# Kernel optimization log

Measured on AMD Instinct MI355X. Metric: run time of the kernel, lower is better.

## Reference

```python
import jax, jax.numpy as jnp
import numpy as np
import math

N_WIRES = 8  # fixed by _QuantumHead; embed_dim == n_wires == 8
NUM_HEADS = 4
HEAD_DIM = N_WIRES // NUM_HEADS


def _apply_cnot(state, ctrl, tgt):
    # state: (N, 2,2,...,2); wire w lives on axis w+1.
    c_ax, t_ax = ctrl + 1, tgt + 1
    s0 = jax.lax.index_in_dim(state, 0, c_ax, keepdims=True)
    s1 = jax.lax.index_in_dim(state, 1, c_ax, keepdims=True)
    s1 = jnp.flip(s1, axis=t_ax)  # flip target where control == 1
    return jnp.concatenate([s0, s1], axis=c_ax)


def quantum_head(x_flat, theta):
    """Batched statevector sim of the _QuantumHead circuit.
    x_flat: (N, 8) rx encoding angles; theta: (8,) trainable RX params.
    RX(x_i) then RX(theta_i) on the same wire compose to RX(x_i + theta_i).
    Returns PauliZ expectations per wire: (N, 8).
    """
    n = x_flat.shape[0]
    state = jnp.zeros((n,) + (2,) * N_WIRES, jnp.complex64)
    state = state.at[(slice(None),) + (0,) * N_WIRES].set(1.0)  # |0...0>
    ang = (x_flat + theta[None, :]) * 0.5
    c, s = jnp.cos(ang), jnp.sin(ang)
    for w in range(N_WIRES):
        ax = w + 1
        a0 = jax.lax.index_in_dim(state, 0, ax, keepdims=False)
        a1 = jax.lax.index_in_dim(state, 1, ax, keepdims=False)
        bshape = (-1,) + (1,) * (N_WIRES - 1)
        cw = c[:, w].reshape(bshape)
        sw = s[:, w].reshape(bshape)
        n0 = cw * a0 - 1j * sw * a1
        n1 = -1j * sw * a0 + cw * a1
        state = jnp.stack([n0, n1], axis=ax)
    for w in range(N_WIRES - 1):
        state = _apply_cnot(state, w, w + 1)
    state = _apply_cnot(state, N_WIRES - 1, 0)
    probs = jnp.real(state * jnp.conj(state))
    outs = []
    for w in range(N_WIRES):
        axes = tuple(a for a in range(1, N_WIRES + 1) if a != w + 1)
        zz = probs.sum(axis=axes)  # (N, 2)
        outs.append(zz[:, 0] - zz[:, 1])
    return jnp.stack(outs, axis=-1)


def setup_inputs() -> dict:
    key = jax.random.key(0)
    k1, k2, k3 = jax.random.split(key, 3)
    B, S, E = 16, 1024, N_WIRES
    x = jax.random.normal(k1, (B, S, E), dtype=jnp.float32)
    mask = jnp.ones((B, S), dtype=jnp.int32)
    theta = jax.random.normal(k2, (E,), dtype=jnp.float32)
    w_out = jax.random.normal(k3, (E, E), dtype=jnp.float32) * (1.0 / math.sqrt(E))
    return {"x": x, "mask": mask, "theta": theta, "w_out": w_out}


def reference(x, mask, theta, w_out):
    B, S, E = x.shape
    # q, k, v are all _apply_quantum(x) with shared parameters -> identical.
    qkv = quantum_head(x.reshape(B * S, E), theta).reshape(B, S, E)
    h = qkv.reshape(B, S, NUM_HEADS, HEAD_DIM).transpose(0, 2, 1, 3)  # (B,H,S,d)
    scores = jnp.einsum("bhqd,bhkd->bhqk", h, h) / math.sqrt(HEAD_DIM)
    scores = jnp.where(mask[:, None, None, :] == 0, -jnp.inf, scores)
    attn = jax.nn.softmax(scores, axis=-1)  # dropout is identity in eval
    out = jnp.einsum("bhqk,bhkd->bhqd", attn, h)
    out = out.transpose(0, 2, 1, 3).reshape(B, S, E)
    return out @ w_out.T
```

## Files before the change

### kernel.cpp

```cpp
#include <hip/hip_runtime.h>

#define BB 16
#define SS 1024
#define NW 8
#define QB 64
#define PS 1032

typedef float v2f __attribute__((ext_vector_type(2)));

__global__ __launch_bounds__(1024)
void mhaq_kernel(const float* __restrict__ x,
                 const int*   __restrict__ mask,
                 const float* __restrict__ theta,
                 const float* __restrict__ wout,
                 float* __restrict__ out)
{
    __shared__ float P[8 * PS];
    __shared__ float Qf[QB][NW];
    __shared__ float O[QB][NW];
    __shared__ float W[NW * NW];

    const int tid = threadIdx.x;
    const int b   = blockIdx.x >> 4;
    const int qc  = blockIdx.x & 15;

    float th[NW];
#pragma unroll
    for (int e = 0; e < NW; ++e) th[e] = theta[e];

    {
        const float* xr = x + ((size_t)b * SS + tid) * NW;
        const float4 r0 = *reinterpret_cast<const float4*>(xr);
        const float4 r1 = *reinterpret_cast<const float4*>(xr + 4);
        float g[NW];
        g[0] = __cosf(r0.x + th[0]); g[1] = __cosf(r0.y + th[1]);
        g[2] = __cosf(r0.z + th[2]); g[3] = __cosf(r0.w + th[3]);
        g[4] = __cosf(r1.x + th[4]); g[5] = __cosf(r1.y + th[5]);
        g[6] = __cosf(r1.z + th[6]); g[7] = __cosf(r1.w + th[7]);
        float h[NW];
        h[1] = g[0] * g[1]; h[2] = h[1] * g[2]; h[3] = h[2] * g[3];
        h[4] = h[3] * g[4]; h[5] = h[4] * g[5]; h[6] = h[5] * g[6];
        h[7] = h[6] * g[7];
        h[0] = (g[1] * g[2]) * (g[3] * g[4]) * ((g[5] * g[6]) * g[7]);
        const float mf = (mask[b * SS + tid] != 0) ? 1.0f : 0.0f;
#pragma unroll
        for (int p = 0; p < 4; ++p) {
            P[p * PS + tid]       = h[2 * p]     * mf;
            P[(4 + p) * PS + tid] = h[2 * p + 1] * mf;
        }
        const int r = tid - qc * QB;
        if ((unsigned)r < (unsigned)QB) {
            const float CF = 0.70710678118654752f * 1.44269504088896340f;
#pragma unroll
            for (int w = 0; w < NW; ++w) Qf[r][w] = h[w] * CF;
        }
        if (tid < NW * NW) W[tid] = wout[tid];
        const int cm = __syncthreads_count(mf == 0.0f);

        const int qg = tid >> 6;
        const int hd = (tid >> 4) & 3;
        const int ks = tid & 15;

        float qu[4], qv[4];
#pragma unroll
        for (int i = 0; i < 4; ++i) {
            qu[i] = Qf[qg * 4 + i][2 * hd];
            qv[i] = Qf[qg * 4 + i][2 * hd + 1];
        }

        v2f vd[4], va0[4], va1[4];
#pragma unroll
        for (int i = 0; i < 4; ++i) { vd[i] = (v2f){0.f, 0.f}; va0[i] = (v2f){0.f, 0.f}; va1[i] = (v2f){0.f, 0.f}; }

        const int base0 = hd * PS + 4 * ks;
#pragma unroll
        for (int t = 0; t < 16; ++t) {
            const int a = base0 + 64 * t;
            const float4 Ur = *reinterpret_cast<const float4*>(&P[a]);
            const float4 Vr = *reinterpret_cast<const float4*>(&P[4 * PS + a]);
            const v2f ulo = (v2f){Ur.x, Ur.y}, uhi = (v2f){Ur.z, Ur.w};
            const v2f vlo = (v2f){Vr.x, Vr.y}, vhi = (v2f){Vr.z, Vr.w};
#pragma unroll
            for (int i = 0; i < 4; ++i) {
                const v2f qup = (v2f){qu[i], qu[i]};
                const v2f qvp = (v2f){qv[i], qv[i]};
                const v2f slo = __builtin_elementwise_fma(qup, ulo, qvp * vlo);
                const v2f shi = __builtin_elementwise_fma(qup, uhi, qvp * vhi);
                const v2f wlo = (v2f){__builtin_amdgcn_exp2f(slo.x), __builtin_amdgcn_exp2f(slo.y)};
                const v2f whi = (v2f){__builtin_amdgcn_exp2f(shi.x), __builtin_amdgcn_exp2f(shi.y)};
                vd[i]  += wlo + whi;
                va0[i] = __builtin_elementwise_fma(wlo, ulo, va0[i]);
                va0[i] = __builtin_elementwise_fma(whi, uhi, va0[i]);
                va1[i] = __builtin_elementwise_fma(wlo, vlo, va1[i]);
                va1[i] = __builtin_elementwise_fma(whi, vhi, va1[i]);
            }
        }

        float dd[4], a0[4], a1[4];
#pragma unroll
        for (int i = 0; i < 4; ++i) {
            dd[i] = vd[i].x + vd[i].y;
            a0[i] = va0[i].x + va0[i].y;
            a1[i] = va1[i].x + va1[i].y;
        }
#pragma unroll
        for (int m = 1; m <= 8; m <<= 1) {
#pragma unroll
            for (int i = 0; i < 4; ++i) {
                dd[i] += __shfl_xor(dd[i], m);
                a0[i] += __shfl_xor(a0[i], m);
                a1[i] += __shfl_xor(a1[i], m);
            }
        }
        if (ks == 0) {
#pragma unroll
            for (int i = 0; i < 4; ++i) {
                const float inv = 1.0f / (dd[i] - (float)cm);
                O[qg * 4 + i][2 * hd]     = a0[i] * inv;
                O[qg * 4 + i][2 * hd + 1] = a1[i] * inv;
            }
        }
    }
    __syncthreads();

    if (tid < QB * NW) {
        const int q = tid >> 3, e = tid & 7;
        float s = 0.f;
#pragma unroll
        for (int f = 0; f < NW; ++f) s = __builtin_fmaf(O[q][f], W[e * NW + f], s);
        out[((size_t)(b * SS + qc * QB + q)) * NW + e] = s;
    }
}

extern "C" void kernel_launch(void* const* d_in, const int* in_sizes, int n_in,
                              void* d_out, int out_size, void* d_ws, size_t ws_size,
                              hipStream_t stream) {
    const float* x     = (const float*)d_in[0];
    const int*   mask  = (const int*)d_in[1];
    const float* theta = (const float*)d_in[2];
    const float* wout  = (const float*)d_in[3];
    float* out = (float*)d_out;

    dim3 grid(BB * (SS / QB));
    dim3 block(1024);
    mhaq_kernel<<<grid, block, 0, stream>>>(x, mask, theta, wout, out);
}
```

Before: 17.76 us.

## Replace per-pair exp softmax with truncated Taylor moment expansion over keys

The exact exp(q·k) softmax is replaced by a degree-8 Taylor expansion of the exponential. This lets each head precompute 55 key-moment sums (powers of u and v, weighted by v components for the numerator) once. Each query then evaluates a small polynomial against those moments, so the per-query-key exp and FMA work is gone. The block shrinks from 1024 to 256 threads with 4 rows per thread. The trade-offs are a truncation error bound that relies on |q·k| staying small (which holds since values are products of cosines), plus extra shuffle reductions and more serial synchronisation stages.

Measured after the change: 15.28 us, median of 2. 14.0% less time.

```diff
diff --git a/kernel.cpp b/kernel.cpp
--- a/kernel.cpp
+++ b/kernel.cpp
@@ -4,32 +4,36 @@
 #define SS 1024
 #define NW 8
 #define QB 64
-#define PS 1032
+#define NH 4
 
-typedef float v2f __attribute__((ext_vector_type(2)));
-
-__global__ __launch_bounds__(1024)
-void mhaq_kernel(const float* __restrict__ x,
-                 const int*   __restrict__ mask,
-                 const float* __restrict__ theta,
-                 const float* __restrict__ wout,
-                 float* __restrict__ out)
+__global__ __launch_bounds__(256)
+void mhaq_one(const float* __restrict__ x, const int* __restrict__ mask,
+              const float* __restrict__ theta, const float* __restrict__ wout,
+              float* __restrict__ out)
 {
-    __shared__ float P[8 * PS];
-    __shared__ float Qf[QB][NW];
-    __shared__ float O[QB][NW];
-    __shared__ float W[NW * NW];
+    __shared__ float2 P[NH][SS];
+    __shared__ float  Qf[QB][NW];
+    __shared__ float  O[QB][NW];
+    __shared__ float  W[64];
+    __shared__ float  Traw[NH][55];
+    __shared__ float  Ts[NH][9][12], Ta[NH][9][12], Tb[NH][9][12];
+    __shared__ int    CMcnt;
 
     const int tid = threadIdx.x;
     const int b   = blockIdx.x >> 4;
     const int qc  = blockIdx.x & 15;
 
+    if (tid == 0) CMcnt = 0;
+
     float th[NW];
 #pragma unroll
     for (int e = 0; e < NW; ++e) th[e] = theta[e];
 
-    {
-        const float* xr = x + ((size_t)b * SS + tid) * NW;
+    int localMasked = 0;
+#pragma unroll
+    for (int c = 0; c < 4; ++c) {
+        const int row = tid + 256 * c;
+        const float* xr = x + ((size_t)b * SS + row) * NW;
         const float4 r0 = *reinterpret_cast<const float4*>(xr);
         const float4 r1 = *reinterpret_cast<const float4*>(xr + 4);
         float g[NW];
@@ -42,93 +46,108 @@
         h[4] = h[3] * g[4]; h[5] = h[4] * g[5]; h[6] = h[5] * g[6];
         h[7] = h[6] * g[7];
         h[0] = (g[1] * g[2]) * (g[3] * g[4]) * ((g[5] * g[6]) * g[7]);
-        const float mf = (mask[b * SS + tid] != 0) ? 1.0f : 0.0f;
+        const float mf = (mask[b * SS + row] != 0) ? 1.0f : 0.0f;
+        localMasked += (mf == 0.0f) ? 1 : 0;
 #pragma unroll
-        for (int p = 0; p < 4; ++p) {
-            P[p * PS + tid]       = h[2 * p]     * mf;
-            P[(4 + p) * PS + tid] = h[2 * p + 1] * mf;
+        for (int hd = 0; hd < NH; ++hd)
+            P[hd][row] = make_float2(h[2 * hd] * mf, h[2 * hd + 1] * mf);
+        const int r = row - qc * QB;
+        if ((unsigned)r < (unsigned)QB) {
+            *reinterpret_cast<float4*>(&Qf[r][0]) = make_float4(h[0], h[1], h[2], h[3]);
+            *reinterpret_cast<float4*>(&Qf[r][4]) = make_float4(h[4], h[5], h[6], h[7]);
         }
-        const int r = tid - qc * QB;
-        if ((unsigned)r < (unsigned)QB) {
-            const float CF = 0.70710678118654752f * 1.44269504088896340f;
+    }
+    if (localMasked) atomicAdd(&CMcnt, localMasked);
+    if (tid < 64) W[tid] = wout[tid];
+    __syncthreads();
+
+    {
+        const int hd = tid >> 6, lane = tid & 63;
+        float acc[55];
 #pragma unroll
-            for (int w = 0; w < NW; ++w) Qf[r][w] = h[w] * CF;
-        }
-        if (tid < NW * NW) W[tid] = wout[tid];
-        const int cm = __syncthreads_count(mf == 0.0f);
-
-        const int qg = tid >> 6;
-        const int hd = (tid >> 4) & 3;
-        const int ks = tid & 15;
-
-        float qu[4], qv[4];
+        for (int m = 1; m < 55; ++m) acc[m] = 0.0f;
+#pragma unroll 4
+        for (int c = 0; c < 16; ++c) {
+            const float2 uv = P[hd][c * 64 + lane];
+            float muj[10], mvi[10];
+            muj[0] = 1.0f; muj[1] = uv.x;
+            mvi[0] = 1.0f; mvi[1] = uv.y;
 #pragma unroll
-        for (int i = 0; i < 4; ++i) {
-            qu[i] = Qf[qg * 4 + i][2 * hd];
-            qv[i] = Qf[qg * 4 + i][2 * hd + 1];
-        }
-
-        v2f vd[4], va0[4], va1[4];
+            for (int j = 2; j <= 9; ++j) { muj[j] = muj[j - 1] * uv.x; mvi[j] = mvi[j - 1] * uv.y; }
 #pragma unroll
-        for (int i = 0; i < 4; ++i) { vd[i] = (v2f){0.f, 0.f}; va0[i] = (v2f){0.f, 0.f}; va1[i] = (v2f){0.f, 0.f}; }
-
-        const int base0 = hd * PS + 4 * ks;
+            for (int s = 1; s <= 9; ++s)
 #pragma unroll
-        for (int t = 0; t < 16; ++t) {
-            const int a = base0 + 64 * t;
-            const float4 Ur = *reinterpret_cast<const float4*>(&P[a]);
-            const float4 Vr = *reinterpret_cast<const float4*>(&P[4 * PS + a]);
-            const v2f ulo = (v2f){Ur.x, Ur.y}, uhi = (v2f){Ur.z, Ur.w};
-            const v2f vlo = (v2f){Vr.x, Vr.y}, vhi = (v2f){Vr.z, Vr.w};
-#pragma unroll
-            for (int i = 0; i < 4; ++i) {
-                const v2f qup = (v2f){qu[i], qu[i]};
-                const v2f qvp = (v2f){qv[i], qv[i]};
-                const v2f slo = __builtin_elementwise_fma(qup, ulo, qvp * vlo);
-                const v2f shi = __builtin_elementwise_fma(qup, uhi, qvp * vhi);
-                const v2f wlo = (v2f){__builtin_amdgcn_exp2f(slo.x), __builtin_amdgcn_exp2f(slo.y)};
-                const v2f whi = (v2f){__builtin_amdgcn_exp2f(shi.x), __builtin_amdgcn_exp2f(shi.y)};
-                vd[i]  += wlo + whi;
-                va0[i] = __builtin_elementwise_fma(wlo, ulo, va0[i]);
-                va0[i] = __builtin_elementwise_fma(whi, uhi, va0[i]);
-                va1[i] = __builtin_elementwise_fma(wlo, vlo, va1[i]);
-                va1[i] = __builtin_elementwise_fma(whi, vhi, va1[i]);
-            }
-        }
-
-        float dd[4], a0[4], a1[4];
-#pragma unroll
-        for (int i = 0; i < 4; ++i) {
-            dd[i] = vd[i].x + vd[i].y;
-            a0[i] = va0[i].x + va0[i].y;
-            a1[i] = va1[i].x + va1[i].y;
+                for (int j = 0; j <= s; ++j)
+                    acc[s * (s + 1) / 2 + j] =
+                        __builtin_fmaf(muj[j], mvi[s - j], acc[s * (s + 1) / 2 + j]);
         }
 #pragma unroll
-        for (int m = 1; m <= 8; m <<= 1) {
+        for (int st = 1; st <= 32; st <<= 1)
 #pragma unroll
-            for (int i = 0; i < 4; ++i) {
-                dd[i] += __shfl_xor(dd[i], m);
-                a0[i] += __shfl_xor(a0[i], m);
-                a1[i] += __shfl_xor(a1[i], m);
-            }
-        }
-        if (ks == 0) {
+            for (int m = 1; m < 55; ++m) acc[m] += __shfl_xor(acc[m], st);
+        if (lane == 0) {
+            Traw[hd][0] = (float)(SS - CMcnt);
 #pragma unroll
-            for (int i = 0; i < 4; ++i) {
-                const float inv = 1.0f / (dd[i] - (float)cm);
-                O[qg * 4 + i][2 * hd]     = a0[i] * inv;
-                O[qg * 4 + i][2 * hd + 1] = a1[i] * inv;
-            }
+            for (int m = 1; m < 55; ++m) Traw[hd][m] = acc[m];
         }
     }
     __syncthreads();
 
-    if (tid < QB * NW) {
-        const int q = tid >> 3, e = tid & 7;
-        float s = 0.f;
+    if (tid < NH * 45) {
+        const int hh = tid / 45;
+        int mm = tid % 45, s = 0;
+        while (mm > s) { mm -= s + 1; ++s; }
+        const int j = mm, i = s - mm;
+        float fj = 1.0f, fi = 1.0f;
+        for (int t = 2; t <= j; ++t) fj *= (float)t;
+        for (int t = 2; t <= i; ++t) fi *= (float)t;
+        const float invf = 1.0f / (fj * fi);
+        const int id0 = s * (s + 1) / 2 + j;
+        const int ida = (s + 1) * (s + 2) / 2 + (j + 1);
+        const int idb = (s + 1) * (s + 2) / 2 + j;
+        Ts[hh][j][i] = Traw[hh][id0] * invf;
+        Ta[hh][j][i] = Traw[hh][ida] * invf;
+        Tb[hh][j][i] = Traw[hh][idb] * invf;
+    }
+    __syncthreads();
+
+    {
+        const int q  = tid >> 2;
+        const int hh = tid & 3;
+        const float CF = 0.70710678118654752f;
+        const float qfu = Qf[q][2 * hh] * CF;
+        const float qfv = Qf[q][2 * hh + 1] * CF;
+        float pu[9], pv[9];
+        pu[0] = 1.0f; pv[0] = 1.0f;
 #pragma unroll
-        for (int f = 0; f < NW; ++f) s = __builtin_fmaf(O[q][f], W[e * NW + f], s);
-        out[((size_t)(b * SS + qc * QB + q)) * NW + e] = s;
+        for (int j = 1; j <= 8; ++j) { pu[j] = pu[j - 1] * qfu; pv[j] = pv[j - 1] * qfv; }
+        float d = 0.0f, a0 = 0.0f, a1 = 0.0f;
+#pragma unroll
+        for (int s = 0; s <= 8; ++s)
+#pragma unroll
+            for (int j = 0; j <= s; ++j) {
+                const float base = pu[j] * pv[s - j];
+                d  = __builtin_fmaf(base, Ts[hh][j][s - j], d);
+                a0 = __builtin_fmaf(base, Ta[hh][j][s - j], a0);
+                a1 = __builtin_fmaf(base, Tb[hh][j][s - j], a1);
+            }
+        const float inv = 1.0f / d;
+        O[q][2 * hh]     = a0 * inv;
+        O[q][2 * hh + 1] = a1 * inv;
+    }
+    __syncthreads();
+
+    {
+        const int q  = tid >> 2;
+        const int ep = tid & 3;
+        float s0 = 0.0f, s1 = 0.0f;
+#pragma unroll
+        for (int f = 0; f < NW; ++f) {
+            s0 = __builtin_fmaf(O[q][f], W[(2 * ep) * NW + f], s0);
+            s1 = __builtin_fmaf(O[q][f], W[(2 * ep + 1) * NW + f], s1);
+        }
+        float* op = out + ((size_t)(b * SS + qc * QB + q)) * NW + 2 * ep;
+        *reinterpret_cast<float2*>(op) = make_float2(s0, s1);
     }
 }
 
@@ -141,7 +160,5 @@
     const float* wout  = (const float*)d_in[3];
     float* out = (float*)d_out;
 
-    dim3 grid(BB * (SS / QB));
-    dim3 block(1024);
-    mhaq_kernel<<<grid, block, 0, stream>>>(x, mask, theta, wout, out);
+    mhaq_one<<<dim3(BB * (SS / QB)), dim3(256), 0, stream>>>(x, mask, theta, wout, out);
 }
```
